# Kernel optimization log

Hardware: AMD Instinct MI355X
Metric: run time of the kernel (lower is better)

Reference implementation:

```python
import jax, jax.numpy as jnp
import numpy as np

N = 1536       # number of agents in the group
T = 20         # track length (only last step used)
H = 64         # hidden_size
E = 16         # embadding_size
M = 128        # PNMLP_hidden_size


def setup_inputs() -> dict:
    key = jax.random.key(0)
    ks = jax.random.split(key, 8)
    s = lambda fan_in: 1.0 / np.sqrt(fan_in)
    return {
        "hidden_state": jax.random.normal(ks[0], (N, H), dtype=jnp.float32),
        "group_track": jax.random.normal(ks[1], (N, T, 2), dtype=jnp.float32),
        "We": jax.random.uniform(ks[2], (2, E), jnp.float32, -s(2), s(2)),
        "be": jax.random.uniform(ks[3], (E,), jnp.float32, -s(2), s(2)),
        "W1": jax.random.uniform(ks[4], (E + H, M), jnp.float32, -s(E + H), s(E + H)),
        "b1": jax.random.uniform(ks[5], (M,), jnp.float32, -s(E + H), s(E + H)),
        "W2": jax.random.uniform(ks[6], (M, H), jnp.float32, -s(M), s(M)),
        "b2": jax.random.uniform(ks[7], (H,), jnp.float32, -s(M), s(M)),
    }


def reference(hidden_state, group_track, We, be, W1, b1, W2, b2):
    # end positions of every track: [N, 2]
    end = group_track[:, -1, :]
    # rel[i, j] = end[j] - end[i]  (neighbor j relative to center i): [N, N, 2]
    rel = end[None, :, :] - end[:, None, :]
    # linear embedding of relative end positions: [N, N, E]
    emb = rel @ We + be
    # concat hidden state (same for all centers) with embedding: [N, N, E+H]
    h = jnp.broadcast_to(hidden_state[None, :, :], (rel.shape[0], rel.shape[1], hidden_state.shape[1]))
    x = jnp.concatenate((h, emb), axis=-1)
    # MLP [E+H -> M -> H] with ReLU after each linear (batch_norm=False)
    x = jax.nn.relu(x @ W1 + b1)
    x = jax.nn.relu(x @ W2 + b2)
    # max-pool over neighbors j for each center i: [N, H]
    return jnp.max(x, axis=1)
```

## Files before the change

kernel.cpp:

```cpp
#include <hip/hip_runtime.h>


#define NN 1536
#define HH 64
#define EE 16
#define MM 128
#define TT 20

#define NI 3
#define NIGRP (NN / NI)
#define JSPLIT 4
#define NTILE (96 / JSPLIT)
#define HTILE (NTILE / 2)

typedef _Float16 half8 __attribute__((ext_vector_type(8)));
typedef float f32x4 __attribute__((ext_vector_type(4)));

__global__ __launch_bounds__(128) void precompute_kernel(
    const float* __restrict__ hidden, const float* __restrict__ gt,
    const float* __restrict__ We, const float* __restrict__ be,
    const float* __restrict__ W1, const float* __restrict__ b1,
    const float* __restrict__ W2,
    _Float16* __restrict__ Qf, _Float16* __restrict__ P,
    _Float16* __restrict__ W2f, float* __restrict__ out)
{
  const int j = blockIdx.x;
  const int m = threadIdx.x;
  const float* hrow = hidden + j * HH;
  float a0 = 0.f, a1 = 0.f;
  #pragma unroll 8
  for (int h = 0; h < HH; h += 2) {
    a0 = fmaf(hrow[h],     W1[h * MM + m],       a0);
    a1 = fmaf(hrow[h + 1], W1[(h + 1) * MM + m], a1);
  }
  const float a = a0 + a1;
  float ve0 = 0.f, ve1 = 0.f, cm = b1[m];
  #pragma unroll
  for (int e = 0; e < EE; ++e) {
    float w1e = W1[(HH + e) * MM + m];
    ve0 = fmaf(We[e], w1e, ve0);
    ve1 = fmaf(We[EE + e], w1e, ve1);
    cm  = fmaf(be[e], w1e, cm);
  }
  const float e0 = gt[j * (2 * TT) + 2 * (TT - 1)];
  const float e1 = gt[j * (2 * TT) + 2 * (TT - 1) + 1];
  const float p = fmaf(e0, ve0, e1 * ve1);
  P[j * MM + m] = (_Float16)p;

  const int jt = j >> 4;
  const int ks = m >> 5;
  const int ln = ((m >> 3) & 3) * 16 + (j & 15);
  const int jj = m & 7;
  Qf[(((jt * 4) + ks) * 64 + ln) * 8 + jj] = (_Float16)(a + p + cm);

  if (m < HH) out[j * HH + m] = 0.f;

  if (j < 8) {
    const int u = j * 128 + m;
    const int ct = u >> 8;
    const int ksx = (u >> 6) & 3;
    const int l = u & 63;
    half8 w;
    #pragma unroll
    for (int t = 0; t < 8; ++t)
      w[t] = (_Float16)W2[(ksx * 32 + (l >> 4) * 8 + t) * HH + ct * 16 + (l & 15)];
    *(half8*)(W2f + (size_t)u * 8) = w;
  }
}

__global__ __launch_bounds__(64, 2) void pairmlp_max_kernel(
    const _Float16* __restrict__ Qf, const _Float16* __restrict__ P,
    const _Float16* __restrict__ W2f, const float* __restrict__ b2,
    float* __restrict__ out)
{
  const int lane = threadIdx.x;
  const int quad = lane >> 4;
  const int lcol = lane & 15;
  const int ig = blockIdx.x % NIGRP;
  const int js = blockIdx.x / NIGRP;
  const int i0 = ig * NI;
  const int par = blockIdx.x & 1;

  half8 bfrag[4][4];
  {
    const half8* wf = (const half8*)W2f + lane;
    #pragma unroll
    for (int ct = 0; ct < 4; ++ct)
      #pragma unroll
      for (int ks = 0; ks < 4; ++ks)
        bfrag[ct][ks] = wf[(ct * 4 + ks) * 64];
  }

  half8 pv[NI][4];
  #pragma unroll
  for (int ii = 0; ii < NI; ++ii) {
    const _Float16* prow = P + (i0 + ii) * MM + quad * 8;
    #pragma unroll
    for (int ks = 0; ks < 4; ++ks)
      pv[ii][ks] = *(const half8*)(prow + ks * 32);
  }

  float b2v[4];
  #pragma unroll
  for (int ct = 0; ct < 4; ++ct) b2v[ct] = b2[ct * 16 + lcol];

  float rmax[NI][4];
  #pragma unroll
  for (int ii = 0; ii < NI; ++ii)
    #pragma unroll
    for (int ct = 0; ct < 4; ++ct) rmax[ii][ct] = -3.0e38f;

  const char* qbytes = (const char*)Qf + (size_t)(js * NTILE) * 4096 + lane * 16;

  const half8 hz = 0;

  auto compute_tile = [&](const half8* qt) {
    f32x4 acc[NI][4];
    #pragma unroll
    for (int ks = 0; ks < 4; ++ks) {
      __builtin_amdgcn_s_setprio(1);
      #pragma unroll
      for (int ii = 0; ii < NI; ++ii) {
        half8 s = qt[ks] - pv[ii][ks];
        s = __builtin_elementwise_max(s, hz);
        #pragma unroll
        for (int ct = 0; ct < 4; ++ct) {
          if (ks == 0)
            acc[ii][ct] = __builtin_amdgcn_mfma_f32_16x16x32_f16(
                s, bfrag[ct][0], f32x4{0.f, 0.f, 0.f, 0.f}, 0, 0, 0);
          else
            acc[ii][ct] = __builtin_amdgcn_mfma_f32_16x16x32_f16(
                s, bfrag[ct][ks], acc[ii][ct], 0, 0, 0);
        }
      }
      __builtin_amdgcn_s_setprio(0);
    }
    #pragma unroll
    for (int ii = 0; ii < NI; ++ii)
      #pragma unroll
      for (int ct = 0; ct < 4; ++ct) {
        const float t3 = fmaxf(fmaxf(acc[ii][ct][0], acc[ii][ct][1]), acc[ii][ct][2]);
        rmax[ii][ct] = fmaxf(fmaxf(t3, acc[ii][ct][3]), rmax[ii][ct]);
      }
  };

  half8 qc[4], qn[4];

  for (int h = 0; h < 2; ++h) {
    const char* runb = qbytes + (((h ^ par) != 0) ? HTILE * 4096 : 0);
    const char* qp = runb;

    #pragma unroll
    for (int ks = 0; ks < 4; ++ks)
      qc[ks] = *(const half8*)(qp + ks * 1024);

    for (int t = 0; t < HTILE; t += 2) {
      #pragma unroll
      for (int ks = 0; ks < 4; ++ks)
        qn[ks] = *(const half8*)(qp + 4096 + ks * 1024);
      compute_tile(qc);

      const char* q2 = (t + 2 < HTILE) ? (qp + 8192) : runb;
      #pragma unroll
      for (int ks = 0; ks < 4; ++ks)
        qc[ks] = *(const half8*)(q2 + ks * 1024);
      compute_tile(qn);

      qp += 8192;
    }
  }

  #pragma unroll
  for (int ii = 0; ii < NI; ++ii)
    #pragma unroll
    for (int ct = 0; ct < 4; ++ct) {
      float v = rmax[ii][ct];
      v = fmaxf(v, __shfl_xor(v, 16, 64));
      v = fmaxf(v, __shfl_xor(v, 32, 64));
      v = fmaxf(v + b2v[ct], 0.f);
      if (quad == 0)
        atomicMax((unsigned*)(out + (i0 + ii) * HH + ct * 16 + lcol), __float_as_uint(v));
    }
}

extern "C" void kernel_launch(void* const* d_in, const int* in_sizes, int n_in,
                              void* d_out, int out_size, void* d_ws, size_t ws_size,
                              hipStream_t stream) {
  const float* hidden = (const float*)d_in[0];
  const float* gt     = (const float*)d_in[1];
  const float* We     = (const float*)d_in[2];
  const float* be     = (const float*)d_in[3];
  const float* W1     = (const float*)d_in[4];
  const float* b1     = (const float*)d_in[5];
  const float* W2     = (const float*)d_in[6];
  const float* b2     = (const float*)d_in[7];
  float* out = (float*)d_out;

  _Float16* Qf  = (_Float16*)d_ws;
  _Float16* Ph  = Qf + NN * MM;
  _Float16* W2f = Ph + NN * MM;

  precompute_kernel<<<NN, 128, 0, stream>>>(hidden, gt, We, be, W1, b1, W2, Qf, Ph, W2f, out);
  pairmlp_max_kernel<<<NIGRP * JSPLIT, 64, 0, stream>>>(Qf, Ph, W2f, b2, out);
}
```

Measured before the change: 103.0 us.

## Split output columns across blocks and software-pipeline max reduction with double accumulators

Each block now handles only two of the four 16-column output tiles, doubling the grid, which halves the B-fragment and accumulator registers per block. The max reduction of the previous tile's accumulators is interleaved into the next tile's MFMA sequence through ping-pong accumulator sets, so the VALU reductions can overlap matrix work. The parity-based half-run ordering is dropped in favour of one linear sweep. The cost is that the relu-subtract on Q-P, which does not depend on the output columns, is now computed twice across the column-split blocks, and there are twice as many atomics.

```diff
diff --git a/kernel.cpp b/kernel.cpp
--- a/kernel.cpp
+++ b/kernel.cpp
@@ -10,8 +10,8 @@
 #define NI 3
 #define NIGRP (NN / NI)
 #define JSPLIT 4
+#define CSPL 2
 #define NTILE (96 / JSPLIT)
-#define HTILE (NTILE / 2)
 
 typedef _Float16 half8 __attribute__((ext_vector_type(8)));
 typedef float f32x4 __attribute__((ext_vector_type(4)));
@@ -77,18 +77,19 @@
   const int quad = lane >> 4;
   const int lcol = lane & 15;
   const int ig = blockIdx.x % NIGRP;
-  const int js = blockIdx.x / NIGRP;
+  const int rest = blockIdx.x / NIGRP;
+  const int js = rest & (JSPLIT - 1);
+  const int cs = rest >> 2;
   const int i0 = ig * NI;
-  const int par = blockIdx.x & 1;
-
-  half8 bfrag[4][4];
+
+  half8 bfrag[2][4];
   {
     const half8* wf = (const half8*)W2f + lane;
     #pragma unroll
-    for (int ct = 0; ct < 4; ++ct)
+    for (int c = 0; c < 2; ++c)
       #pragma unroll
       for (int ks = 0; ks < 4; ++ks)
-        bfrag[ct][ks] = wf[(ct * 4 + ks) * 64];
+        bfrag[c][ks] = wf[((cs * 2 + c) * 4 + ks) * 64];
   }
 
   half8 pv[NI][4];
@@ -100,22 +101,29 @@
       pv[ii][ks] = *(const half8*)(prow + ks * 32);
   }
 
-  float b2v[4];
-  #pragma unroll
-  for (int ct = 0; ct < 4; ++ct) b2v[ct] = b2[ct * 16 + lcol];
-
-  float rmax[NI][4];
-  #pragma unroll
-  for (int ii = 0; ii < NI; ++ii)
-    #pragma unroll
-    for (int ct = 0; ct < 4; ++ct) rmax[ii][ct] = -3.0e38f;
+  float b2v[2];
+  #pragma unroll
+  for (int c = 0; c < 2; ++c) b2v[c] = b2[(cs * 2 + c) * 16 + lcol];
+
+  float rmax[NI][2];
+  #pragma unroll
+  for (int ii = 0; ii < NI; ++ii)
+    #pragma unroll
+    for (int c = 0; c < 2; ++c) rmax[ii][c] = -3.0e38f;
 
   const char* qbytes = (const char*)Qf + (size_t)(js * NTILE) * 4096 + lane * 16;
 
   const half8 hz = 0;
-
-  auto compute_tile = [&](const half8* qt) {
-    f32x4 acc[NI][4];
+  const f32x4 fz = {0.f, 0.f, 0.f, 0.f};
+  const f32x4 fninf = {-3.0e38f, -3.0e38f, -3.0e38f, -3.0e38f};
+
+  f32x4 accA[NI][2], accB[NI][2];
+  #pragma unroll
+  for (int ii = 0; ii < NI; ++ii)
+    #pragma unroll
+    for (int c = 0; c < 2; ++c) accB[ii][c] = fninf;
+
+  auto tile = [&](f32x4 (&acc)[NI][2], f32x4 (&oacc)[NI][2], const half8 (&qt)[4]) {
     #pragma unroll
     for (int ks = 0; ks < 4; ++ks) {
       __builtin_amdgcn_s_setprio(1);
@@ -123,63 +131,67 @@
       for (int ii = 0; ii < NI; ++ii) {
         half8 s = qt[ks] - pv[ii][ks];
         s = __builtin_elementwise_max(s, hz);
-        #pragma unroll
-        for (int ct = 0; ct < 4; ++ct) {
-          if (ks == 0)
-            acc[ii][ct] = __builtin_amdgcn_mfma_f32_16x16x32_f16(
-                s, bfrag[ct][0], f32x4{0.f, 0.f, 0.f, 0.f}, 0, 0, 0);
-          else
-            acc[ii][ct] = __builtin_amdgcn_mfma_f32_16x16x32_f16(
-                s, bfrag[ct][ks], acc[ii][ct], 0, 0, 0);
+        if (ks == 0) {
+          acc[ii][0] = __builtin_amdgcn_mfma_f32_16x16x32_f16(s, bfrag[0][0], fz, 0, 0, 0);
+          acc[ii][1] = __builtin_amdgcn_mfma_f32_16x16x32_f16(s, bfrag[1][0], fz, 0, 0, 0);
+        } else {
+          acc[ii][0] = __builtin_amdgcn_mfma_f32_16x16x32_f16(s, bfrag[0][ks], acc[ii][0], 0, 0, 0);
+          acc[ii][1] = __builtin_amdgcn_mfma_f32_16x16x32_f16(s, bfrag[1][ks], acc[ii][1], 0, 0, 0);
         }
       }
       __builtin_amdgcn_s_setprio(0);
+      if (ks >= 1) {
+        const int di = ks - 1;
+        #pragma unroll
+        for (int c = 0; c < 2; ++c) {
+          const float t3 = fmaxf(fmaxf(oacc[di][c][0], oacc[di][c][1]), oacc[di][c][2]);
+          rmax[di][c] = fmaxf(fmaxf(t3, oacc[di][c][3]), rmax[di][c]);
+        }
+      }
     }
-    #pragma unroll
-    for (int ii = 0; ii < NI; ++ii)
-      #pragma unroll
-      for (int ct = 0; ct < 4; ++ct) {
-        const float t3 = fmaxf(fmaxf(acc[ii][ct][0], acc[ii][ct][1]), acc[ii][ct][2]);
-        rmax[ii][ct] = fmaxf(fmaxf(t3, acc[ii][ct][3]), rmax[ii][ct]);
-      }
   };
 
   half8 qc[4], qn[4];
-
-  for (int h = 0; h < 2; ++h) {
-    const char* runb = qbytes + (((h ^ par) != 0) ? HTILE * 4096 : 0);
-    const char* qp = runb;
-
+  const char* qp = qbytes;
+
+  #pragma unroll
+  for (int ks = 0; ks < 4; ++ks)
+    qc[ks] = *(const half8*)(qp + ks * 1024);
+
+  for (int t = 0; t < NTILE; t += 2) {
     #pragma unroll
     for (int ks = 0; ks < 4; ++ks)
-      qc[ks] = *(const half8*)(qp + ks * 1024);
-
-    for (int t = 0; t < HTILE; t += 2) {
-      #pragma unroll
-      for (int ks = 0; ks < 4; ++ks)
-        qn[ks] = *(const half8*)(qp + 4096 + ks * 1024);
-      compute_tile(qc);
-
-      const char* q2 = (t + 2 < HTILE) ? (qp + 8192) : runb;
-      #pragma unroll
-      for (int ks = 0; ks < 4; ++ks)
-        qc[ks] = *(const half8*)(q2 + ks * 1024);
-      compute_tile(qn);
-
-      qp += 8192;
+      qn[ks] = *(const half8*)(qp + 4096 + ks * 1024);
+    tile(accA, accB, qc);
+
+    const char* q2 = (t + 2 < NTILE) ? (qp + 8192) : qbytes;
+    #pragma unroll
+    for (int ks = 0; ks < 4; ++ks)
+      qc[ks] = *(const half8*)(q2 + ks * 1024);
+    tile(accB, accA, qn);
+
+    qp += 8192;
+  }
+
+  #pragma unroll
+  for (int ii = 0; ii < NI; ++ii)
+    #pragma unroll
+    for (int c = 0; c < 2; ++c) {
+      const float t3 = fmaxf(fmaxf(accB[ii][c][0], accB[ii][c][1]), accB[ii][c][2]);
+      rmax[ii][c] = fmaxf(fmaxf(t3, accB[ii][c][3]), rmax[ii][c]);
     }
-  }
-
-  #pragma unroll
-  for (int ii = 0; ii < NI; ++ii)
-    #pragma unroll
-    for (int ct = 0; ct < 4; ++ct) {
-      float v = rmax[ii][ct];
+
+  #pragma unroll
+  for (int ii = 0; ii < NI; ++ii)
+    #pragma unroll
+    for (int c = 0; c < 2; ++c) {
+      float v = rmax[ii][c];
       v = fmaxf(v, __shfl_xor(v, 16, 64));
       v = fmaxf(v, __shfl_xor(v, 32, 64));
-      v = fmaxf(v + b2v[ct], 0.f);
+      v = fmaxf(v + b2v[c], 0.f);
       if (quad == 0)
-        atomicMax((unsigned*)(out + (i0 + ii) * HH + ct * 16 + lcol), __float_as_uint(v));
+        atomicMax((unsigned*)(out + (i0 + ii) * HH + (cs * 2 + c) * 16 + lcol),
+                  __float_as_uint(v));
     }
 }
 
@@ -201,5 +213,5 @@
   _Float16* W2f = Ph + NN * MM;
 
   precompute_kernel<<<NN, 128, 0, stream>>>(hidden, gt, We, be, W1, b1, W2, Qf, Ph, W2f, out);
-  pairmlp_max_kernel<<<NIGRP * JSPLIT, 64, 0, stream>>>(Qf, Ph, W2f, b2, out);
+  pairmlp_max_kernel<<<NIGRP * JSPLIT * CSPL, 64, 0, stream>>>(Qf, Ph, W2f, b2, out);
 }
```

New measurement: 116.9 us. 1.13x slower.
